# Kernel tuning notes

Measured on AMD Instinct MI355X. Metric: run time of the kernel, lower is better.

The kernel has to match this reference:

```python
import jax, jax.numpy as jnp
import numpy as np

# Model hyper-parameters (from CMRET __init__ defaults)
N_A, F, H, K, NK, L = 4096, 128, 4, 15, 50, 6
CUTOFF, TEMP, BOX, N_Z = 5.0, 2.0, 40.0, 100
DH = F // H  # per-head dim


def setup_inputs() -> dict:
    key = jax.random.key(0)
    ks = jax.random.split(key, 12)
    Z = jax.random.randint(ks[0], (1, N_A), 0, N_Z)
    R = jax.random.uniform(ks[1], (1, N_A, 3), dtype=jnp.float32) * BOX
    batch = jnp.ones((1, N_A, 1), jnp.float32)
    g = lambda k, shp, s: jax.random.normal(k, shp, jnp.float32) * s
    emb = g(ks[2], (N_Z, F), 1.0)
    Wq = g(ks[3], (L, F, F), F ** -0.5)
    Wk = g(ks[4], (L, F, F), F ** -0.5)
    Wv = g(ks[5], (L, F, 3 * F), F ** -0.5)
    We_k = g(ks[6], (L, NK, F), NK ** -0.5)
    be_k = jnp.zeros((L, F), jnp.float32)
    We_v = g(ks[7], (L, NK, 3 * F), NK ** -0.5)
    be_v = jnp.zeros((L, 3 * F), jnp.float32)
    ln_g = jnp.ones((F,), jnp.float32)
    ln_b = jnp.zeros((F,), jnp.float32)
    Wo1 = g(ks[8], (F, F), F ** -0.5)
    Wo2 = g(ks[9], (F, 1), F ** -0.5)
    return dict(Z=Z, R=R, batch=batch, emb=emb, Wq=Wq, Wk=Wk, Wv=Wv,
                We_k=We_k, be_k=be_k, We_v=We_v, be_v=be_v,
                ln_g=ln_g, ln_b=ln_b, Wo1=Wo1, Wo2=Wo2)


def reference(Z, R, batch, emb, Wq, Wk, Wv, We_k, be_k, We_v, be_v, ln_g, ln_b, Wo1, Wo2):
    n_a = Z.shape[1]
    r = R[0]                                  # (n_a, 3)
    b = batch[..., 0]                         # (1, n_a)
    bm = (b.T @ b) == 0                       # (n_a, n_a) cross-molecule mask
    # --- Distance: k-nearest-neighbour selection (gather-based) ---
    sq = jnp.sum(r * r, -1)
    d2 = sq[:, None] + sq[None, :] - 2.0 * (r @ r.T)
    d2 = jnp.where(bm | jnp.eye(n_a, dtype=bool), 1e9, jnp.maximum(d2, 0.0))
    _, idxs = jax.lax.top_k(-d2, K)           # (n_a, K) neighbour indices
    vec = r[idxs] - r[:, None, :]             # (n_a, K, 3)
    d = jnp.sqrt(jnp.sum(vec * vec, -1) + 1e-12)
    vec_norm = vec / d[..., None]
    # --- Gaussian RBF * cosine cutoff edge features ---
    mu = jnp.linspace(0.0, CUTOFF, NK, dtype=jnp.float32)
    delta = CUTOFF / NK
    cut = 0.5 * (jnp.cos(jnp.pi * d / CUTOFF) + 1.0) * (d <= CUTOFF)
    e = jnp.exp(-((d[..., None] - mu) ** 2) / (2.0 * delta * delta)) * cut[..., None]
    # --- embedding and channel init ---
    s = emb[Z[0]]                             # (n_a, F) scalar channel
    o = jnp.zeros_like(s)                     # residual accumulator
    v = jnp.zeros((n_a, 3, F), s.dtype)       # vector channel
    scale = jnp.asarray(1.0 / np.sqrt(DH * TEMP), jnp.float32)
    # --- attention interaction stack ---
    for l in range(L):
        q = (s @ Wq[l]).reshape(n_a, H, DH)
        kk = s @ Wk[l]
        val = s @ Wv[l]                       # (n_a, 3F)
        ek = jax.nn.silu(e @ We_k[l] + be_k[l])   # (n_a, K, F) edge key filter
        ev = jax.nn.silu(e @ We_v[l] + be_v[l])   # (n_a, K, 3F) edge value filter
        kh = (kk[idxs] * ek).reshape(n_a, K, H, DH)
        logits = jnp.einsum('nhd,nkhd->nkh', q, kh) * scale
        attn = jax.nn.softmax(logits, axis=1) * cut[..., None]
        wf = jnp.repeat(attn, DH, axis=-1)        # (n_a, K, F) per-channel weights
        m1, m2, m3 = jnp.split(val[idxs] * ev, 3, axis=-1)
        ds = jnp.sum(wf * m1, axis=1)             # scalar message (n_a, F)
        dv = jnp.sum((wf * m2)[:, :, None, :] * vec_norm[..., None]
                     + (wf * m3)[:, :, None, :] * v[idxs], axis=1)
        s = s + ds
        o = o + ds
        v = v + dv
    # --- final LayerNorm + readout ---
    mean = o.mean(-1, keepdims=True)
    var = o.var(-1, keepdims=True)
    o = (o - mean) / jnp.sqrt(var + 1e-5) * ln_g + ln_b
    h = jax.nn.silu(o @ Wo1) @ Wo2            # (n_a, 1) per-atom contribution
    return jnp.sum(h * batch[0], axis=0, keepdims=True)  # (1, 1) energy
```

## Files before the change

### kernel.cpp

```cpp
#include <hip/hip_runtime.h>
#include <math.h>

#define NATOMS 4096
#define FDIM   128
#define NHEAD  4
#define DHEAD  32
#define KNBR   15
#define NKER   50
#define NLAYER 6
#define QKVW   640

typedef __attribute__((ext_vector_type(8))) short short8;
typedef __attribute__((ext_vector_type(4))) float f32x4;

__device__ __forceinline__ float silu_f(float x) { return x / (1.0f + __expf(-x)); }

__device__ __forceinline__ unsigned long long shfl_xor_u64(unsigned long long v, int m) {
    unsigned lo = (unsigned)v, hi = (unsigned)(v >> 32);
    lo = (unsigned)__shfl_xor((int)lo, m);
    hi = (unsigned)__shfl_xor((int)hi, m);
    return ((unsigned long long)hi << 32) | lo;
}
__device__ __forceinline__ unsigned long long min_u64(unsigned long long a, unsigned long long b) {
    return a < b ? a : b;
}

__global__ __launch_bounds__(256) void knn_kernel(
    const float* __restrict__ R, const float* __restrict__ batch,
    int* __restrict__ idxs, float* __restrict__ cutw,
    float* __restrict__ vecn, float* __restrict__ ebuf)
{
    __shared__ float d2s[NATOMS];
    __shared__ unsigned long long wred[2][4];
    __shared__ int sel[KNBR];
    const int i = blockIdx.x, t = threadIdx.x;
    const int wave = t >> 6, lane = t & 63;
    const float xi = R[i*3+0], yi = R[i*3+1], zi = R[i*3+2];
    const float bi = batch[i];
    const float sqi = xi*xi + yi*yi + zi*zi;
    for (int j = t; j < NATOMS; j += 256) {
        float xj = R[j*3+0], yj = R[j*3+1], zj = R[j*3+2];
        float sqj = xj*xj + yj*yj + zj*zj;
        float d2 = sqi + sqj - 2.0f*(xi*xj + yi*yj + zi*zj);
        if (bi*batch[j] == 0.0f || j == i) d2 = 1e9f;
        else d2 = fmaxf(d2, 0.0f);
        d2s[j] = d2;
    }
    __syncthreads();

    unsigned long long cand = ~0ull;
    #pragma unroll
    for (int it = 0; it < 16; ++it) {
        int j = t + it*256;
        unsigned long long p = ((unsigned long long)__float_as_uint(d2s[j]) << 32) | (unsigned)j;
        cand = min_u64(cand, p);
    }
    for (int k = 0; k < KNBR; ++k) {
        unsigned long long w = cand;
        #pragma unroll
        for (int off = 1; off < 64; off <<= 1)
            w = min_u64(w, shfl_xor_u64(w, off));
        if (lane == 0) wred[k & 1][wave] = w;
        __syncthreads();
        unsigned long long f = min_u64(min_u64(wred[k&1][0], wred[k&1][1]),
                                       min_u64(wred[k&1][2], wred[k&1][3]));
        int sj = (int)(unsigned)f;
        if (t == 0) sel[k] = sj;
        if ((sj & 255) == t) {
            d2s[sj] = 1e9f;
            cand = ~0ull;
            #pragma unroll
            for (int it = 0; it < 16; ++it) {
                int j = t + it*256;
                unsigned long long p = ((unsigned long long)__float_as_uint(d2s[j]) << 32) | (unsigned)j;
                cand = min_u64(cand, p);
            }
        }
    }
    __syncthreads();

    if (t < KNBR) {
        int j = sel[t];
        idxs[i*KNBR + t] = j;
        float vx = R[j*3+0]-xi, vy = R[j*3+1]-yi, vz = R[j*3+2]-zi;
        float d = sqrtf(vx*vx + vy*vy + vz*vz + 1e-12f);
        float inv = 1.0f/d;
        vecn[(i*KNBR+t)*3+0] = vx*inv;
        vecn[(i*KNBR+t)*3+1] = vy*inv;
        vecn[(i*KNBR+t)*3+2] = vz*inv;
        const float PI = 3.14159265358979323846f;
        float cutv = (d <= 5.0f) ? 0.5f*(cosf(PI*d*0.2f) + 1.0f) : 0.0f;
        cutw[i*KNBR + t] = cutv;
        for (int jj = 0; jj < NKER; ++jj) {
            float mu = 5.0f * (float)jj / 49.0f;
            float dd = d - mu;
            ebuf[(i*KNBR+t)*NKER + jj] = __expf(-dd*dd*50.0f) * cutv;
        }
    }
}

__global__ __launch_bounds__(256) void init_kernel(
    const int* __restrict__ Z, const float* __restrict__ emb,
    float* __restrict__ s, float* __restrict__ o, float* __restrict__ v0)
{
    int stride = gridDim.x * blockDim.x;
    for (int idx = blockIdx.x*blockDim.x + threadIdx.x; idx < NATOMS*3*FDIM; idx += stride) {
        v0[idx] = 0.0f;
        if (idx < NATOMS*FDIM) {
            int a = idx >> 7, c = idx & 127;
            s[idx] = emb[Z[a]*FDIM + c];
            o[idx] = 0.0f;
        }
    }
}

__global__ __launch_bounds__(64) void wprep_kernel(
    const float* __restrict__ WeK, const float* __restrict__ WeV,
    unsigned short* __restrict__ Wswz)
{
    const int blk = blockIdx.x;
    const int lane = threadIdx.x;
    const int ks = blk & 1;
    const int T  = (blk >> 1) & 31;
    const int l  = blk >> 6;
    const int quad = lane >> 4, x = lane & 15;
    unsigned short* dst = Wswz + (size_t)blk*1024 + lane*8;
    for (int j = 0; j < 8; ++j) {
        int k = ks*32 + quad*8 + j;
        float w = 0.0f;
        if (k < NKER)
            w = (T < 8) ? WeK[l*NKER*FDIM + k*FDIM + T*16 + x]
                        : WeV[(size_t)l*NKER*3*FDIM + k*3*FDIM + (T-8)*16 + x];
        unsigned b = __float_as_uint(w);
        dst[j] = (unsigned short)(b >> 16);
        float r = w - __uint_as_float(b & 0xFFFF0000u);
        dst[512 + j] = (unsigned short)(__float_as_uint(r) >> 16);
    }
}

__global__ __launch_bounds__(64) void qprep_kernel(
    const float* __restrict__ Wq, const float* __restrict__ Wk,
    const float* __restrict__ Wv, unsigned short* __restrict__ Qswz)
{
    const int blk = blockIdx.x;
    const int lane = threadIdx.x;
    const int ks = blk & 3;
    const int ct = (blk >> 2) % 40;
    const int l  = blk / 160;
    const int quad = lane >> 4, lx = lane & 15;
    const int col = ct*16 + lx;
    unsigned short* dst = Qswz + (size_t)blk*1024 + lane*8;
    for (int j = 0; j < 8; ++j) {
        int k = ks*32 + quad*8 + j;
        float w;
        if (col < 128)      w = Wq[l*16384 + k*128 + col];
        else if (col < 256) w = Wk[l*16384 + k*128 + (col-128)];
        else                w = Wv[(size_t)l*49152 + k*384 + (col-256)];
        unsigned b = __float_as_uint(w);
        dst[j] = (unsigned short)(b >> 16);
        float r = w - __uint_as_float(b & 0xFFFF0000u);
        dst[512 + j] = (unsigned short)(__float_as_uint(r) >> 16);
    }
}

__global__ __launch_bounds__(128) void proj_kernel(
    const float* __restrict__ S, const unsigned short* __restrict__ Qswz,
    float* __restrict__ QKV, int l)
{
    const int rt = blockIdx.x;
    const int t = threadIdx.x, wave = t >> 6, lane = t & 63;
    const int quad = lane >> 4, lx = lane & 15;
    const int cg = blockIdx.y*2 + wave;

    short8 ah[4], al[4];
    const float* srow = S + (size_t)(rt*16 + lx)*FDIM;
    #pragma unroll
    for (int ks = 0; ks < 4; ++ks) {
        float v[8];
        *(f32x4*)&v[0] = *(const f32x4*)(srow + ks*32 + quad*8);
        *(f32x4*)&v[4] = *(const f32x4*)(srow + ks*32 + quad*8 + 4);
        #pragma unroll
        for (int j = 0; j < 8; ++j) {
            unsigned b = __float_as_uint(v[j]);
            ah[ks][j] = (short)(b >> 16);
            float r = v[j] - __uint_as_float(b & 0xFFFF0000u);
            al[ks][j] = (short)(__float_as_uint(r) >> 16);
        }
    }
    for (int ci = 0; ci < 10; ++ci) {
        const int ct = cg*10 + ci;
        const unsigned short* wp = Qswz + (size_t)((l*40 + ct)*4)*1024 + lane*8;
        f32x4 acc = {0.0f, 0.0f, 0.0f, 0.0f};
        #pragma unroll
        for (int ks = 0; ks < 4; ++ks) {
            short8 bh = *(const short8*)(wp + ks*1024);
            short8 bl = *(const short8*)(wp + ks*1024 + 512);
            acc = __builtin_amdgcn_mfma_f32_16x16x32_bf16(ah[ks], bh, acc, 0, 0, 0);
            acc = __builtin_amdgcn_mfma_f32_16x16x32_bf16(ah[ks], bl, acc, 0, 0, 0);
            acc = __builtin_amdgcn_mfma_f32_16x16x32_bf16(al[ks], bh, acc, 0, 0, 0);
        }
        const int col = ct*16 + lx;
        #pragma unroll
        for (int r = 0; r < 4; ++r)
            QKV[(size_t)(rt*16 + quad*4 + r)*QKVW + col] = acc[r];
    }
}

__global__ __launch_bounds__(512) void attn_kernel(
    const float* __restrict__ QKV, const int* __restrict__ idxs,
    const float* __restrict__ cutw, const float* __restrict__ vecn,
    const float* __restrict__ ebuf, const unsigned short* __restrict__ Wswz,
    const float* __restrict__ beK, const float* __restrict__ beV,
    float* __restrict__ s, float* __restrict__ o,
    const float* __restrict__ vin, float* __restrict__ vout, int l)
{
    __shared__ __align__(16) float es[16][68];
    __shared__ float fbuf[KNBR][516];
    __shared__ int   nidx[KNBR];
    __shared__ float cutv[KNBR];
    __shared__ float vnc[KNBR][3];
    __shared__ float attns[KNBR][NHEAD];
    __shared__ float dvbuf[3][FDIM];

    const int i = blockIdx.x, t = threadIdx.x;
    const int wave = t >> 6, lane = t & 63;
    const int quad = lane >> 4, lx = lane & 15;

    if (t < KNBR) {
        nidx[t] = idxs[i*KNBR + t];
        cutv[t] = cutw[i*KNBR + t];
        vnc[t][0] = vecn[(i*KNBR+t)*3+0];
        vnc[t][1] = vecn[(i*KNBR+t)*3+1];
        vnc[t][2] = vecn[(i*KNBR+t)*3+2];
    }
    for (int x = t; x < 16*64; x += 512) {
        int row = x >> 6, col = x & 63;
        es[row][col] = (row < KNBR && col < NKER)
                       ? ebuf[(size_t)i*KNBR*NKER + row*NKER + col] : 0.0f;
    }
    __syncthreads();

    short8 eh[2], el[2];
    #pragma unroll
    for (int ks = 0; ks < 2; ++ks) {
        float v[8];
        *(f32x4*)&v[0] = *(const f32x4*)&es[lx][ks*32 + quad*8];
        *(f32x4*)&v[4] = *(const f32x4*)&es[lx][ks*32 + quad*8 + 4];
        #pragma unroll
        for (int j = 0; j < 8; ++j) {
            unsigned b = __float_as_uint(v[j]);
            eh[ks][j] = (short)(b >> 16);
            float r = v[j] - __uint_as_float(b & 0xFFFF0000u);
            el[ks][j] = (short)(__float_as_uint(r) >> 16);
        }
    }

    #pragma unroll
    for (int tt = 0; tt < 4; ++tt) {
        const int T = wave*4 + tt;
        const int col = T*16 + lx;
        f32x4 acc = {0.0f, 0.0f, 0.0f, 0.0f};
        #pragma unroll
        for (int ks = 0; ks < 2; ++ks) {
            const unsigned short* wp = Wswz + ((size_t)((l*32+T)*2+ks))*1024 + lane*8;
            short8 bh = *(const short8*)wp;
            short8 bl = *(const short8*)(wp + 512);
            acc = __builtin_amdgcn_mfma_f32_16x16x32_bf16(eh[ks], bh, acc, 0, 0, 0);
            acc = __builtin_amdgcn_mfma_f32_16x16x32_bf16(eh[ks], bl, acc, 0, 0, 0);
            acc = __builtin_amdgcn_mfma_f32_16x16x32_bf16(el[ks], bh, acc, 0, 0, 0);
        }
        const float b = (col < FDIM) ? beK[l*FDIM + col]
                                     : beV[(size_t)l*3*FDIM + (col - FDIM)];
        const int goff = (col < FDIM) ? (FDIM + col) : (2*FDIM + (col - FDIM));
        #pragma unroll
        for (int r = 0; r < 4; ++r) {
            int k = quad*4 + r;
            if (k < KNBR) {
                float f = silu_f(acc[r] + b);
                float g = QKV[(size_t)nidx[k]*QKVW + goff];
                fbuf[k][col] = f * g;
            }
        }
    }
    __syncthreads();

    if (t < FDIM) {
        const int c = t, h = c >> 5;
        const float q = QKV[(size_t)i*QKVW + c];
        float lg[KNBR];
        #pragma unroll
        for (int k = 0; k < KNBR; ++k) {
            float p = q * fbuf[k][c];
            p += __shfl_xor(p, 1);
            p += __shfl_xor(p, 2);
            p += __shfl_xor(p, 4);
            p += __shfl_xor(p, 8);
            p += __shfl_xor(p, 16);
            lg[k] = p * 0.125f;
        }
        float m = -1e30f;
        #pragma unroll
        for (int k = 0; k < KNBR; ++k) m = fmaxf(m, lg[k]);
        float ssum = 0.0f;
        #pragma unroll
        for (int k = 0; k < KNBR; ++k) { lg[k] = __expf(lg[k]-m); ssum += lg[k]; }
        float inv = 1.0f/ssum;
        if ((c & 31) == 0) {
            #pragma unroll
            for (int k = 0; k < KNBR; ++k) attns[k][h] = lg[k]*inv*cutv[k];
        }
    }
    float mval[KNBR];
    int cv = 0, h2 = 0;
    if (t >= FDIM) {
        cv = t - FDIM; h2 = (cv & 127) >> 5;
        #pragma unroll
        for (int k = 0; k < KNBR; ++k) mval[k] = fbuf[k][FDIM + cv];
    }
    __syncthreads();

    if (t >= FDIM) {
        if (cv < FDIM) {
            float ds = 0.0f;
            #pragma unroll
            for (int k = 0; k < KNBR; ++k) ds += attns[k][h2]*mval[k];
            s[i*FDIM + cv] += ds;
            o[i*FDIM + cv] += ds;
        } else if (cv < 2*FDIM) {
            const int cc = cv - FDIM;
            float d0 = 0.0f, d1 = 0.0f, d2 = 0.0f;
            #pragma unroll
            for (int k = 0; k < KNBR; ++k) {
                float w = attns[k][h2]*mval[k];
                d0 += w*vnc[k][0]; d1 += w*vnc[k][1]; d2 += w*vnc[k][2];
            }
            dvbuf[0][cc] = d0; dvbuf[1][cc] = d1; dvbuf[2][cc] = d2;
        }
    }
    float d3[3] = {0.0f, 0.0f, 0.0f};
    if (t >= FDIM && cv >= 2*FDIM) {
        const int cc = cv - 2*FDIM;
        #pragma unroll
        for (int k = 0; k < KNBR; ++k) {
            float w = attns[k][h2]*mval[k];
            const float* vb = vin + (size_t)nidx[k]*3*FDIM + cc;
            d3[0] += w*vb[0*FDIM]; d3[1] += w*vb[1*FDIM]; d3[2] += w*vb[2*FDIM];
        }
    }
    __syncthreads();
    if (t >= FDIM && cv >= 2*FDIM) {
        const int cc = cv - 2*FDIM;
        #pragma unroll
        for (int x = 0; x < 3; ++x) {
            size_t off = (size_t)i*3*FDIM + x*FDIM + cc;
            vout[off] = vin[off] + dvbuf[x][cc] + d3[x];
        }
    }
}

__global__ void zero_kernel(float* out) { out[0] = 0.0f; }

__global__ __launch_bounds__(128) void final_kernel(
    const float* __restrict__ o, const float* __restrict__ lng, const float* __restrict__ lnb,
    const float* __restrict__ Wo1, const float* __restrict__ Wo2,
    const float* __restrict__ batch, float* __restrict__ out)
{
    __shared__ float red[128];
    __shared__ float on[128];
    const int i = blockIdx.x, t = threadIdx.x;
    float x = o[i*FDIM + t];
    red[t] = x; __syncthreads();
    for (int off = 64; off > 0; off >>= 1) { if (t < off) red[t] += red[t+off]; __syncthreads(); }
    float mean = red[0] * (1.0f/128.0f);
    __syncthreads();
    float xm = x - mean;
    red[t] = xm*xm; __syncthreads();
    for (int off = 64; off > 0; off >>= 1) { if (t < off) red[t] += red[t+off]; __syncthreads(); }
    float var = red[0] * (1.0f/128.0f);
    __syncthreads();
    on[t] = xm * rsqrtf(var + 1e-5f) * lng[t] + lnb[t];
    __syncthreads();
    float acc = 0.0f;
    #pragma unroll 8
    for (int j = 0; j < 128; ++j) acc += on[j] * Wo1[j*128 + t];
    float h = silu_f(acc) * Wo2[t];
    red[t] = h; __syncthreads();
    for (int off = 64; off > 0; off >>= 1) { if (t < off) red[t] += red[t+off]; __syncthreads(); }
    if (t == 0) atomicAdd(out, red[0] * batch[i]);
}

extern "C" void kernel_launch(void* const* d_in, const int* in_sizes, int n_in,
                              void* d_out, int out_size, void* d_ws, size_t ws_size,
                              hipStream_t stream)
{
    const int*   Z     = (const int*)  d_in[0];
    const float* R     = (const float*)d_in[1];
    const float* batch = (const float*)d_in[2];
    const float* emb   = (const float*)d_in[3];
    const float* Wq    = (const float*)d_in[4];
    const float* Wk    = (const float*)d_in[5];
    const float* Wv    = (const float*)d_in[6];
    const float* WeK   = (const float*)d_in[7];
    const float* beK   = (const float*)d_in[8];
    const float* WeV   = (const float*)d_in[9];
    const float* beV   = (const float*)d_in[10];
    const float* lng   = (const float*)d_in[11];
    const float* lnb   = (const float*)d_in[12];
    const float* Wo1   = (const float*)d_in[13];
    const float* Wo2   = (const float*)d_in[14];
    float* out = (float*)d_out;

    float* fws = (float*)d_ws;
    float* s    = fws; fws += NATOMS*FDIM;
    float* o    = fws; fws += NATOMS*FDIM;
    float* v0   = fws; fws += NATOMS*3*FDIM;
    float* v1   = fws; fws += NATOMS*3*FDIM;
    float* qkv  = fws; fws += NATOMS*QKVW;
    float* cutw = fws; fws += NATOMS*KNBR;
    float* vecn = fws; fws += NATOMS*KNBR*3;
    float* ebuf = fws; fws += NATOMS*KNBR*NKER;
    int*   idxs = (int*)fws; fws += NATOMS*KNBR;
    unsigned short* Wswz = (unsigned short*)fws;
    fws += (NLAYER*32*2*1024) / 2;
    unsigned short* Qswz = (unsigned short*)fws;

    wprep_kernel<<<NLAYER*32*2, 64, 0, stream>>>(WeK, WeV, Wswz);
    qprep_kernel<<<NLAYER*40*4, 64, 0, stream>>>(Wq, Wk, Wv, Qswz);
    knn_kernel<<<NATOMS, 256, 0, stream>>>(R, batch, idxs, cutw, vecn, ebuf);
    init_kernel<<<1024, 256, 0, stream>>>(Z, emb, s, o, v0);
    for (int l = 0; l < NLAYER; ++l) {
        proj_kernel<<<dim3(256, 2), 128, 0, stream>>>(s, Qswz, qkv, l);
        float* vin  = (l & 1) ? v1 : v0;
        float* vout = (l & 1) ? v0 : v1;
        attn_kernel<<<NATOMS, 512, 0, stream>>>(qkv, idxs, cutw, vecn, ebuf, Wswz,
                                                beK, beV, s, o, vin, vout, l);
    }
    zero_kernel<<<1, 1, 0, stream>>>(out);
    final_kernel<<<NATOMS, 128, 0, stream>>>(o, lng, lnb, Wo1, Wo2, batch, out);
}
```

Baseline: 621.6 us.

## Prefetch neighbor key/value rows into LDS and replace atomic energy sum with reduction

The attention kernel now stages each neighbor's 512 key+value columns from QKV into shared memory with coalesced 16-byte vector loads before the edge-filter MFMA. The epilogue multiplies by the staged value instead of doing scattered scalar global loads per element. Separately, the final readout writes per-atom contributions to a buffer and a single-block kernel reduces them, replacing the zero kernel plus 4096 atomics on one address. This adds an extra barrier in the attention kernel and an extra tiny launch.

```diff
diff --git a/kernel.cpp b/kernel.cpp
--- a/kernel.cpp
+++ b/kernel.cpp
@@ -215,7 +215,7 @@
     const float* __restrict__ vin, float* __restrict__ vout, int l)
 {
     __shared__ __align__(16) float es[16][68];
-    __shared__ float fbuf[KNBR][516];
+    __shared__ __align__(16) float fbuf[KNBR][516];
     __shared__ int   nidx[KNBR];
     __shared__ float cutv[KNBR];
     __shared__ float vnc[KNBR][3];
@@ -240,6 +240,12 @@
     }
     __syncthreads();
 
+    for (int x = t; x < KNBR*128; x += 512) {
+        int k = x >> 7, c4 = x & 127;
+        *(f32x4*)&fbuf[k][c4*4] =
+            *(const f32x4*)(QKV + (size_t)nidx[k]*QKVW + FDIM + c4*4);
+    }
+
     short8 eh[2], el[2];
     #pragma unroll
     for (int ks = 0; ks < 2; ++ks) {
@@ -254,6 +260,7 @@
             el[ks][j] = (short)(__float_as_uint(r) >> 16);
         }
     }
+    __syncthreads();
 
     #pragma unroll
     for (int tt = 0; tt < 4; ++tt) {
@@ -271,14 +278,12 @@
         }
         const float b = (col < FDIM) ? beK[l*FDIM + col]
                                      : beV[(size_t)l*3*FDIM + (col - FDIM)];
-        const int goff = (col < FDIM) ? (FDIM + col) : (2*FDIM + (col - FDIM));
         #pragma unroll
         for (int r = 0; r < 4; ++r) {
             int k = quad*4 + r;
             if (k < KNBR) {
                 float f = silu_f(acc[r] + b);
-                float g = QKV[(size_t)nidx[k]*QKVW + goff];
-                fbuf[k][col] = f * g;
+                fbuf[k][col] = f * fbuf[k][col];
             }
         }
     }
@@ -358,12 +363,10 @@
     }
 }
 
-__global__ void zero_kernel(float* out) { out[0] = 0.0f; }
-
 __global__ __launch_bounds__(128) void final_kernel(
     const float* __restrict__ o, const float* __restrict__ lng, const float* __restrict__ lnb,
     const float* __restrict__ Wo1, const float* __restrict__ Wo2,
-    const float* __restrict__ batch, float* __restrict__ out)
+    const float* __restrict__ batch, float* __restrict__ hout)
 {
     __shared__ float red[128];
     __shared__ float on[128];
@@ -386,7 +389,21 @@
     float h = silu_f(acc) * Wo2[t];
     red[t] = h; __syncthreads();
     for (int off = 64; off > 0; off >>= 1) { if (t < off) red[t] += red[t+off]; __syncthreads(); }
-    if (t == 0) atomicAdd(out, red[0] * batch[i]);
+    if (t == 0) hout[i] = red[0] * batch[i];
+}
+
+__global__ __launch_bounds__(1024) void reduce_kernel(
+    const float* __restrict__ hout, float* __restrict__ out)
+{
+    __shared__ float red[1024];
+    const int t = threadIdx.x;
+    float a = hout[t] + hout[t+1024] + hout[t+2048] + hout[t+3072];
+    red[t] = a; __syncthreads();
+    for (int off = 512; off > 0; off >>= 1) {
+        if (t < off) red[t] += red[t+off];
+        __syncthreads();
+    }
+    if (t == 0) out[0] = red[0];
 }
 
 extern "C" void kernel_launch(void* const* d_in, const int* in_sizes, int n_in,
@@ -419,6 +436,7 @@
     float* cutw = fws; fws += NATOMS*KNBR;
     float* vecn = fws; fws += NATOMS*KNBR*3;
     float* ebuf = fws; fws += NATOMS*KNBR*NKER;
+    float* hout = fws; fws += NATOMS;
     int*   idxs = (int*)fws; fws += NATOMS*KNBR;
     unsigned short* Wswz = (unsigned short*)fws;
     fws += (NLAYER*32*2*1024) / 2;
@@ -435,6 +453,6 @@
         attn_kernel<<<NATOMS, 512, 0, stream>>>(qkv, idxs, cutw, vecn, ebuf, Wswz,
                                                 beK, beV, s, o, vin, vout, l);
     }
-    zero_kernel<<<1, 1, 0, stream>>>(out);
-    final_kernel<<<NATOMS, 128, 0, stream>>>(o, lng, lnb, Wo1, Wo2, batch, out);
-}
+    final_kernel<<<NATOMS, 128, 0, stream>>>(o, lng, lnb, Wo1, Wo2, batch, hout);
+    reduce_kernel<<<1, 1024, 0, stream>>>(hout, out);
+}
```

Result: faster. 587.8 us (-5.4%).
